# Performance work log

Measured on AMD Instinct MI355X. Metric: run time of the kernel, lower is better.

## Reference

```python
import jax, jax.numpy as jnp
import numpy as np

N_NODES = 100000
N_EDGES = 3200000
IN_DIM = 512
HID_DIM = 512


def setup_inputs() -> dict:
    key = jax.random.key(0)
    k = jax.random.split(key, 8)
    x = jax.random.normal(k[0], (N_NODES, IN_DIM), dtype=jnp.float32)
    adj_src = jax.random.randint(k[1], (N_EDGES,), 0, N_NODES, dtype=jnp.int32)
    adj_dst = jax.random.randint(k[2], (N_EDGES,), 0, N_NODES, dtype=jnp.int32)
    adj_val = jax.random.uniform(k[3], (N_EDGES,), dtype=jnp.float32)
    s = 1.0 / np.sqrt(IN_DIM)
    W1 = jax.random.uniform(k[4], (IN_DIM, HID_DIM), minval=-s, maxval=s, dtype=jnp.float32)
    b1 = jnp.zeros((HID_DIM,), dtype=jnp.float32)
    s2 = 1.0 / np.sqrt(HID_DIM)
    W2 = jax.random.uniform(k[5], (HID_DIM, HID_DIM), minval=-s2, maxval=s2, dtype=jnp.float32)
    b2 = jnp.zeros((HID_DIM,), dtype=jnp.float32)
    return {"x": x, "adj_src": adj_src, "adj_dst": adj_dst, "adj_val": adj_val,
            "W1": W1, "b1": b1, "W2": W2, "b2": b2}


def _spmm(src, dst, val, h):
    # adj @ h with adj in COO: out[dst] += val * h[src]
    msgs = h[src] * val[:, None]            # [E, D]
    return jax.ops.segment_sum(msgs, dst, num_segments=N_NODES)


def reference(x, adj_src, adj_dst, adj_val, W1, b1, W2, b2):
    # Inference mode: dropout is identity (training=False).
    # Layer 1: linear -> SpMM -> ReLU
    h = x @ W1 + b1
    h = _spmm(adj_src, adj_dst, adj_val, h)
    h = jax.nn.relu(h)
    # Layer 2: linear -> SpMM -> ReLU
    h = h @ W2 + b2
    h = _spmm(adj_src, adj_dst, adj_val, h)
    h = jax.nn.relu(h)
    return h
```

## Files before the change

kernel.cpp:

```cpp
#include <hip/hip_runtime.h>


#define N_NODES 100000
#define N_EDGES 3200000
#define DIM 512
#define BUCKET_CAP 128

typedef __attribute__((ext_vector_type(8))) __bf16 bf16x8;
typedef __attribute__((ext_vector_type(4))) float f32x4;
typedef __attribute__((ext_vector_type(4))) unsigned int u32x4;

__device__ inline unsigned short f2bf(float f) {
    unsigned int u = __builtin_bit_cast(unsigned int, f);
    unsigned int r = (u + 0x7FFFu + ((u >> 16) & 1u)) >> 16;
    return (unsigned short)r;
}
__device__ inline float bf2f(unsigned short s) {
    unsigned int u = ((unsigned int)s) << 16;
    return __builtin_bit_cast(float, u);
}

__global__ __launch_bounds__(256) void k_cvt(const float4* __restrict__ in,
                                             ushort4* __restrict__ out, int n4) {
    int i = blockIdx.x * 256 + threadIdx.x;
    if (i >= n4) return;
    float4 v = in[i];
    ushort4 o;
    o.x = f2bf(v.x); o.y = f2bf(v.y); o.z = f2bf(v.z); o.w = f2bf(v.w);
    out[i] = o;
}

__global__ __launch_bounds__(256) void k_wt(const float* __restrict__ W,
                                            unsigned short* __restrict__ Wt) {
    int idx = blockIdx.x * 256 + threadIdx.x;
    int k = idx & 511, n = idx >> 9;
    Wt[n * 512 + k] = f2bf(W[k * 512 + n]);
}

__global__ __launch_bounds__(256) void k_scatter(const int* __restrict__ src,
                                                 const int* __restrict__ dst,
                                                 const float* __restrict__ val,
                                                 int* __restrict__ cnt,
                                                 int2* __restrict__ bucket) {
    int e = blockIdx.x * 256 + threadIdx.x;
    if (e >= N_EDGES) return;
    int d = dst[e];
    int pos = atomicAdd(cnt + d, 1);
    if (pos < BUCKET_CAP)
        bucket[((size_t)d << 7) + pos] = make_int2(src[e], __float_as_int(val[e]));
}

__global__ __launch_bounds__(256, 2)
void k_gemm(const unsigned short* __restrict__ A, const unsigned short* __restrict__ Bt,
            const float* __restrict__ bias, unsigned short* __restrict__ C, int M) {
    __shared__ unsigned short sA[128][40];
    __shared__ unsigned short sB[128][40];
    const int t = threadIdx.x;
    const int m0 = blockIdx.x * 128;
    const int n0 = blockIdx.y * 128;
    const int wave = t >> 6;
    const int lane = t & 63;
    const int wm = (wave & 1) << 6;
    const int wn = (wave >> 1) << 6;
    const int quad = lane >> 4;
    const int l16 = lane & 15;

    f32x4 acc[4][4];
#pragma unroll
    for (int i = 0; i < 4; i++)
#pragma unroll
        for (int j = 0; j < 4; j++) acc[i][j] = (f32x4){0.f, 0.f, 0.f, 0.f};

    const int row_s = t >> 2;
    const int q_s = t & 3;

    for (int k0 = 0; k0 < 512; k0 += 32) {
        __syncthreads();
#pragma unroll
        for (int i = 0; i < 2; i++) {
            int row = row_s + (i << 6);
            int gr = m0 + row;
            u32x4 av = {0u, 0u, 0u, 0u};
            if (gr < M) av = *(const u32x4*)(A + (size_t)gr * 512 + k0 + q_s * 8);
            *(u32x4*)(&sA[row][q_s * 8]) = av;
            u32x4 bv = *(const u32x4*)(Bt + (size_t)(n0 + row) * 512 + k0 + q_s * 8);
            *(u32x4*)(&sB[row][q_s * 8]) = bv;
        }
        __syncthreads();
        bf16x8 af[4], bfr[4];
#pragma unroll
        for (int i = 0; i < 4; i++)
            af[i] = *(const bf16x8*)(&sA[wm + i * 16 + l16][quad * 8]);
#pragma unroll
        for (int j = 0; j < 4; j++)
            bfr[j] = *(const bf16x8*)(&sB[wn + j * 16 + l16][quad * 8]);
#pragma unroll
        for (int i = 0; i < 4; i++)
#pragma unroll
            for (int j = 0; j < 4; j++)
                acc[i][j] = __builtin_amdgcn_mfma_f32_16x16x32_bf16(af[i], bfr[j], acc[i][j], 0, 0, 0);
    }

#pragma unroll
    for (int i = 0; i < 4; i++) {
        int rbase = m0 + wm + i * 16 + quad * 4;
#pragma unroll
        for (int j = 0; j < 4; j++) {
            int col = n0 + wn + j * 16 + l16;
            float bv = bias[col];
#pragma unroll
            for (int r = 0; r < 4; r++) {
                int row = rbase + r;
                if (row < M) C[(size_t)row * 512 + col] = f2bf(acc[i][j][r] + bv);
            }
        }
    }
}

__global__ __launch_bounds__(256)
void k_spmm(const int2* __restrict__ bucket, const int* __restrict__ cnt,
            const unsigned short* __restrict__ Hin,
            unsigned short* __restrict__ out_bf, float* __restrict__ out_f32) {
    __shared__ int2 sE[BUCKET_CAP];
    int node = blockIdx.x;
    int t = threadIdx.x;
    int deg = cnt[node];
    if (deg > BUCKET_CAP) deg = BUCKET_CAP;
    if (t < deg) sE[t] = bucket[((size_t)node << 7) + t];
    __syncthreads();
    float ax = 0.f, ay = 0.f;
    for (int e = 0; e < deg; e++) {
        int2 ed = sE[e];
        float v = __int_as_float(ed.y);
        unsigned int p = *(const unsigned int*)(Hin + ((size_t)ed.x << 9) + (t << 1));
        ax += v * bf2f((unsigned short)(p & 0xFFFFu));
        ay += v * bf2f((unsigned short)(p >> 16));
    }
    ax = fmaxf(ax, 0.f);
    ay = fmaxf(ay, 0.f);
    size_t o = ((size_t)node << 9) + (t << 1);
    if (out_f32 != nullptr) {
        float2 st = make_float2(ax, ay);
        *(float2*)(out_f32 + o) = st;
    } else {
        unsigned int pk = (unsigned int)f2bf(ax) | ((unsigned int)f2bf(ay) << 16);
        *(unsigned int*)(out_bf + o) = pk;
    }
}

extern "C" void kernel_launch(void* const* d_in, const int* in_sizes, int n_in,
                              void* d_out, int out_size, void* d_ws, size_t ws_size,
                              hipStream_t stream) {
    const float* x       = (const float*)d_in[0];
    const int*   adj_src = (const int*)d_in[1];
    const int*   adj_dst = (const int*)d_in[2];
    const float* adj_val = (const float*)d_in[3];
    const float* W1      = (const float*)d_in[4];
    const float* b1      = (const float*)d_in[5];
    const float* W2      = (const float*)d_in[6];
    const float* b2      = (const float*)d_in[7];

    const size_t ND = (size_t)N_NODES * DIM;

    unsigned short* xb  = (unsigned short*)d_ws;
    unsigned short* w1t = xb + ND;
    unsigned short* w2t = w1t + 262144;
    int*  cnt    = (int*)(w2t + 262144);
    int2* bucket = (int2*)(cnt + 100096);

    unsigned short* h1 = (unsigned short*)d_out;
    unsigned short* h2 = h1 + ND;
    unsigned short* h3 = xb;

    k_cvt<<<50000, 256, 0, stream>>>((const float4*)x, (ushort4*)xb, (int)(ND / 4));
    k_wt<<<1024, 256, 0, stream>>>(W1, w1t);
    k_wt<<<1024, 256, 0, stream>>>(W2, w2t);

    hipMemsetAsync(cnt, 0, N_NODES * sizeof(int), stream);
    k_scatter<<<12500, 256, 0, stream>>>(adj_src, adj_dst, adj_val, cnt, bucket);

    dim3 ggrid((N_NODES + 127) / 128, 4);

    k_gemm<<<ggrid, 256, 0, stream>>>(xb, w1t, b1, h1, N_NODES);
    k_spmm<<<N_NODES, 256, 0, stream>>>(bucket, cnt, h1, h2, nullptr);

    k_gemm<<<ggrid, 256, 0, stream>>>(h2, w2t, b2, h3, N_NODES);
    k_spmm<<<N_NODES, 256, 0, stream>>>(bucket, cnt, h3, nullptr, (float*)d_out);
}
```

Baseline: 1.700 ms.

## Map one wave per node in SpMM with 16-byte gathers and nontemporal hints

```diff
diff --git a/kernel.cpp b/kernel.cpp
--- a/kernel.cpp
+++ b/kernel.cpp
@@ -9,6 +9,7 @@
 typedef __attribute__((ext_vector_type(8))) __bf16 bf16x8;
 typedef __attribute__((ext_vector_type(4))) float f32x4;
 typedef __attribute__((ext_vector_type(4))) unsigned int u32x4;
+typedef __attribute__((ext_vector_type(2))) int i32x2;
 
 __device__ inline unsigned short f2bf(float f) {
     unsigned int u = __builtin_bit_cast(unsigned int, f);
@@ -20,13 +21,13 @@
     return __builtin_bit_cast(float, u);
 }
 
-__global__ __launch_bounds__(256) void k_cvt(const float4* __restrict__ in,
+__global__ __launch_bounds__(256) void k_cvt(const f32x4* __restrict__ in,
                                              ushort4* __restrict__ out, int n4) {
     int i = blockIdx.x * 256 + threadIdx.x;
     if (i >= n4) return;
-    float4 v = in[i];
+    f32x4 v = __builtin_nontemporal_load(in + i);
     ushort4 o;
-    o.x = f2bf(v.x); o.y = f2bf(v.y); o.z = f2bf(v.z); o.w = f2bf(v.w);
+    o.x = f2bf(v[0]); o.y = f2bf(v[1]); o.z = f2bf(v[2]); o.w = f2bf(v[3]);
     out[i] = o;
 }
 
@@ -41,13 +42,17 @@
                                                  const int* __restrict__ dst,
                                                  const float* __restrict__ val,
                                                  int* __restrict__ cnt,
-                                                 int2* __restrict__ bucket) {
+                                                 i32x2* __restrict__ bucket) {
     int e = blockIdx.x * 256 + threadIdx.x;
     if (e >= N_EDGES) return;
     int d = dst[e];
     int pos = atomicAdd(cnt + d, 1);
-    if (pos < BUCKET_CAP)
-        bucket[((size_t)d << 7) + pos] = make_int2(src[e], __float_as_int(val[e]));
+    if (pos < BUCKET_CAP) {
+        i32x2 ed;
+        ed[0] = src[e];
+        ed[1] = __float_as_int(val[e]);
+        __builtin_nontemporal_store(ed, bucket + ((size_t)d << 7) + pos);
+    }
 }
 
 __global__ __launch_bounds__(256, 2)
@@ -56,8 +61,8 @@
     __shared__ unsigned short sA[128][40];
     __shared__ unsigned short sB[128][40];
     const int t = threadIdx.x;
-    const int m0 = blockIdx.x * 128;
-    const int n0 = blockIdx.y * 128;
+    const int m0 = blockIdx.y * 128;
+    const int n0 = blockIdx.x * 128;
     const int wave = t >> 6;
     const int lane = t & 63;
     const int wm = (wave & 1) << 6;
@@ -118,33 +123,61 @@
 }
 
 __global__ __launch_bounds__(256)
-void k_spmm(const int2* __restrict__ bucket, const int* __restrict__ cnt,
+void k_spmm(const i32x2* __restrict__ bucket, const int* __restrict__ cnt,
             const unsigned short* __restrict__ Hin,
             unsigned short* __restrict__ out_bf, float* __restrict__ out_f32) {
-    __shared__ int2 sE[BUCKET_CAP];
-    int node = blockIdx.x;
-    int t = threadIdx.x;
+    __shared__ i32x2 sE[4][BUCKET_CAP];
+    const int w = threadIdx.x >> 6;
+    const int lane = threadIdx.x & 63;
+    const int node = blockIdx.x * 4 + w;
     int deg = cnt[node];
     if (deg > BUCKET_CAP) deg = BUCKET_CAP;
-    if (t < deg) sE[t] = bucket[((size_t)node << 7) + t];
+    const i32x2* bk = bucket + ((size_t)node << 7);
+    if (lane < deg)      sE[w][lane]      = __builtin_nontemporal_load(bk + lane);
+    if (lane + 64 < deg) sE[w][lane + 64] = __builtin_nontemporal_load(bk + lane + 64);
     __syncthreads();
-    float ax = 0.f, ay = 0.f;
-    for (int e = 0; e < deg; e++) {
-        int2 ed = sE[e];
-        float v = __int_as_float(ed.y);
-        unsigned int p = *(const unsigned int*)(Hin + ((size_t)ed.x << 9) + (t << 1));
-        ax += v * bf2f((unsigned short)(p & 0xFFFFu));
-        ay += v * bf2f((unsigned short)(p >> 16));
-    }
-    ax = fmaxf(ax, 0.f);
-    ay = fmaxf(ay, 0.f);
-    size_t o = ((size_t)node << 9) + (t << 1);
+
+    float a[8];
+#pragma unroll
+    for (int i = 0; i < 8; i++) a[i] = 0.f;
+
+    if (deg > 0) {
+        i32x2 ed = sE[w][0];
+        float v = __int_as_float(ed[1]);
+        u32x4 p = *(const u32x4*)(Hin + (((size_t)ed[0]) << 9) + (lane << 3));
+        for (int e = 1; e < deg; e++) {
+            i32x2 edn = sE[w][e];
+            float vn = __int_as_float(edn[1]);
+            u32x4 pn = *(const u32x4*)(Hin + (((size_t)edn[0]) << 9) + (lane << 3));
+#pragma unroll
+            for (int q = 0; q < 4; q++) {
+                a[2 * q]     += v * __builtin_bit_cast(float, p[q] << 16);
+                a[2 * q + 1] += v * __builtin_bit_cast(float, p[q] & 0xFFFF0000u);
+            }
+            p = pn; v = vn;
+        }
+#pragma unroll
+        for (int q = 0; q < 4; q++) {
+            a[2 * q]     += v * __builtin_bit_cast(float, p[q] << 16);
+            a[2 * q + 1] += v * __builtin_bit_cast(float, p[q] & 0xFFFF0000u);
+        }
+    }
+
+#pragma unroll
+    for (int i = 0; i < 8; i++) a[i] = fmaxf(a[i], 0.f);
+
+    size_t o = (((size_t)node) << 9) + (lane << 3);
     if (out_f32 != nullptr) {
-        float2 st = make_float2(ax, ay);
-        *(float2*)(out_f32 + o) = st;
+        f32x4 v0 = {a[0], a[1], a[2], a[3]};
+        f32x4 v1 = {a[4], a[5], a[6], a[7]};
+        __builtin_nontemporal_store(v0, (f32x4*)(out_f32 + o));
+        __builtin_nontemporal_store(v1, (f32x4*)(out_f32 + o + 4));
     } else {
-        unsigned int pk = (unsigned int)f2bf(ax) | ((unsigned int)f2bf(ay) << 16);
-        *(unsigned int*)(out_bf + o) = pk;
+        u32x4 pk;
+#pragma unroll
+        for (int q = 0; q < 4; q++)
+            pk[q] = (unsigned int)f2bf(a[2 * q]) | ((unsigned int)f2bf(a[2 * q + 1]) << 16);
+        __builtin_nontemporal_store(pk, (u32x4*)(out_bf + o));
     }
 }
 
@@ -166,24 +199,24 @@
     unsigned short* w1t = xb + ND;
     unsigned short* w2t = w1t + 262144;
     int*  cnt    = (int*)(w2t + 262144);
-    int2* bucket = (int2*)(cnt + 100096);
+    i32x2* bucket = (i32x2*)(cnt + 100096);
 
     unsigned short* h1 = (unsigned short*)d_out;
     unsigned short* h2 = h1 + ND;
     unsigned short* h3 = xb;
 
-    k_cvt<<<50000, 256, 0, stream>>>((const float4*)x, (ushort4*)xb, (int)(ND / 4));
+    k_cvt<<<50000, 256, 0, stream>>>((const f32x4*)x, (ushort4*)xb, (int)(ND / 4));
     k_wt<<<1024, 256, 0, stream>>>(W1, w1t);
     k_wt<<<1024, 256, 0, stream>>>(W2, w2t);
 
     hipMemsetAsync(cnt, 0, N_NODES * sizeof(int), stream);
     k_scatter<<<12500, 256, 0, stream>>>(adj_src, adj_dst, adj_val, cnt, bucket);
 
-    dim3 ggrid((N_NODES + 127) / 128, 4);
+    dim3 ggrid(4, (N_NODES + 127) / 128);
 
     k_gemm<<<ggrid, 256, 0, stream>>>(xb, w1t, b1, h1, N_NODES);
-    k_spmm<<<N_NODES, 256, 0, stream>>>(bucket, cnt, h1, h2, nullptr);
+    k_spmm<<<N_NODES / 4, 256, 0, stream>>>(bucket, cnt, h1, h2, nullptr);
 
     k_gemm<<<ggrid, 256, 0, stream>>>(h2, w2t, b2, h3, N_NODES);
-    k_spmm<<<N_NODES, 256, 0, stream>>>(bucket, cnt, h3, nullptr, (float*)d_out);
-}
+    k_spmm<<<N_NODES / 4, 256, 0, stream>>>(bucket, cnt, h3, nullptr, (float*)d_out);
+}
```

Result: slower. 1.766 ms (+3.9%).

## Fuse fp32-to-bf16 conversion into GEMM loads and double-buffer LDS tiles

Applied to the files above, without the earlier changes.

```diff
diff --git a/kernel.cpp b/kernel.cpp
--- a/kernel.cpp
+++ b/kernel.cpp
@@ -19,15 +19,8 @@
     unsigned int u = ((unsigned int)s) << 16;
     return __builtin_bit_cast(float, u);
 }
-
-__global__ __launch_bounds__(256) void k_cvt(const float4* __restrict__ in,
-                                             ushort4* __restrict__ out, int n4) {
-    int i = blockIdx.x * 256 + threadIdx.x;
-    if (i >= n4) return;
-    float4 v = in[i];
-    ushort4 o;
-    o.x = f2bf(v.x); o.y = f2bf(v.y); o.z = f2bf(v.z); o.w = f2bf(v.w);
-    out[i] = o;
+__device__ inline unsigned int pk2(float a, float b) {
+    return (unsigned int)f2bf(a) | ((unsigned int)f2bf(b) << 16);
 }
 
 __global__ __launch_bounds__(256) void k_wt(const float* __restrict__ W,
@@ -50,14 +43,15 @@
         bucket[((size_t)d << 7) + pos] = make_int2(src[e], __float_as_int(val[e]));
 }
 
+template <int AF32>
 __global__ __launch_bounds__(256, 2)
-void k_gemm(const unsigned short* __restrict__ A, const unsigned short* __restrict__ Bt,
+void k_gemm(const void* __restrict__ Ap, const unsigned short* __restrict__ Bt,
             const float* __restrict__ bias, unsigned short* __restrict__ C, int M) {
-    __shared__ unsigned short sA[128][40];
-    __shared__ unsigned short sB[128][40];
+    __shared__ unsigned short sA[2][128][40];
+    __shared__ unsigned short sB[2][128][40];
     const int t = threadIdx.x;
-    const int m0 = blockIdx.x * 128;
-    const int n0 = blockIdx.y * 128;
+    const int m0 = blockIdx.y * 128;
+    const int n0 = blockIdx.x * 128;
     const int wave = t >> 6;
     const int lane = t & 63;
     const int wm = (wave & 1) << 6;
@@ -73,32 +67,73 @@
 
     const int row_s = t >> 2;
     const int q_s = t & 3;
+    const int eo = q_s * 8;
+
+    const int gr0 = m0 + row_s;
+    const int gr1 = m0 + row_s + 64;
+    const bool ok0 = gr0 < M, ok1 = gr1 < M;
+    const unsigned short* __restrict__ pB0 = Bt + (size_t)(n0 + row_s) * 512 + eo;
+    const unsigned short* __restrict__ pB1 = pB0 + (size_t)64 * 512;
+    const u32x4 zz = (u32x4){0u, 0u, 0u, 0u};
+
+    u32x4 rA0, rA1, rB0, rB1;
+
+    auto ld = [&](int k) {
+        if constexpr (AF32) {
+            const float* A = (const float*)Ap;
+            float4 x0 = {0, 0, 0, 0}, x1 = {0, 0, 0, 0};
+            float4 y0 = {0, 0, 0, 0}, y1 = {0, 0, 0, 0};
+            if (ok0) {
+                const float4* q = (const float4*)(A + (size_t)gr0 * 512 + eo + k);
+                x0 = q[0]; x1 = q[1];
+            }
+            if (ok1) {
+                const float4* q = (const float4*)(A + (size_t)gr1 * 512 + eo + k);
+                y0 = q[0]; y1 = q[1];
+            }
+            rA0[0] = pk2(x0.x, x0.y); rA0[1] = pk2(x0.z, x0.w);
+            rA0[2] = pk2(x1.x, x1.y); rA0[3] = pk2(x1.z, x1.w);
+            rA1[0] = pk2(y0.x, y0.y); rA1[1] = pk2(y0.z, y0.w);
+            rA1[2] = pk2(y1.x, y1.y); rA1[3] = pk2(y1.z, y1.w);
+        } else {
+            const unsigned short* A = (const unsigned short*)Ap;
+            rA0 = ok0 ? *(const u32x4*)(A + (size_t)gr0 * 512 + eo + k) : zz;
+            rA1 = ok1 ? *(const u32x4*)(A + (size_t)gr1 * 512 + eo + k) : zz;
+        }
+        rB0 = *(const u32x4*)(pB0 + k);
+        rB1 = *(const u32x4*)(pB1 + k);
+    };
+    auto st = [&](int buf) {
+        *(u32x4*)(&sA[buf][row_s][eo]) = rA0;
+        *(u32x4*)(&sA[buf][row_s + 64][eo]) = rA1;
+        *(u32x4*)(&sB[buf][row_s][eo]) = rB0;
+        *(u32x4*)(&sB[buf][row_s + 64][eo]) = rB1;
+    };
+
+    ld(0);
+    st(0);
+    ld(32);
+    __syncthreads();
 
     for (int k0 = 0; k0 < 512; k0 += 32) {
-        __syncthreads();
-#pragma unroll
-        for (int i = 0; i < 2; i++) {
-            int row = row_s + (i << 6);
-            int gr = m0 + row;
-            u32x4 av = {0u, 0u, 0u, 0u};
-            if (gr < M) av = *(const u32x4*)(A + (size_t)gr * 512 + k0 + q_s * 8);
-            *(u32x4*)(&sA[row][q_s * 8]) = av;
-            u32x4 bv = *(const u32x4*)(Bt + (size_t)(n0 + row) * 512 + k0 + q_s * 8);
-            *(u32x4*)(&sB[row][q_s * 8]) = bv;
-        }
-        __syncthreads();
+        const int cur = (k0 >> 5) & 1;
         bf16x8 af[4], bfr[4];
 #pragma unroll
         for (int i = 0; i < 4; i++)
-            af[i] = *(const bf16x8*)(&sA[wm + i * 16 + l16][quad * 8]);
+            af[i] = *(const bf16x8*)(&sA[cur][wm + i * 16 + l16][quad * 8]);
 #pragma unroll
         for (int j = 0; j < 4; j++)
-            bfr[j] = *(const bf16x8*)(&sB[wn + j * 16 + l16][quad * 8]);
+            bfr[j] = *(const bf16x8*)(&sB[cur][wn + j * 16 + l16][quad * 8]);
 #pragma unroll
         for (int i = 0; i < 4; i++)
 #pragma unroll
             for (int j = 0; j < 4; j++)
                 acc[i][j] = __builtin_amdgcn_mfma_f32_16x16x32_bf16(af[i], bfr[j], acc[i][j], 0, 0, 0);
+        if (k0 + 32 < 512) {
+            st(cur ^ 1);
+            if (k0 + 64 < 512) ld(k0 + 64);
+            __syncthreads();
+        }
     }
 
 #pragma unroll
@@ -172,18 +207,17 @@
     unsigned short* h2 = h1 + ND;
     unsigned short* h3 = xb;
 
-    k_cvt<<<50000, 256, 0, stream>>>((const float4*)x, (ushort4*)xb, (int)(ND / 4));
     k_wt<<<1024, 256, 0, stream>>>(W1, w1t);
     k_wt<<<1024, 256, 0, stream>>>(W2, w2t);
 
     hipMemsetAsync(cnt, 0, N_NODES * sizeof(int), stream);
     k_scatter<<<12500, 256, 0, stream>>>(adj_src, adj_dst, adj_val, cnt, bucket);
 
-    dim3 ggrid((N_NODES + 127) / 128, 4);
-
-    k_gemm<<<ggrid, 256, 0, stream>>>(xb, w1t, b1, h1, N_NODES);
+    dim3 ggrid(4, (N_NODES + 127) / 128);
+
+    k_gemm<1><<<ggrid, 256, 0, stream>>>((const void*)x, w1t, b1, h1, N_NODES);
     k_spmm<<<N_NODES, 256, 0, stream>>>(bucket, cnt, h1, h2, nullptr);
 
-    k_gemm<<<ggrid, 256, 0, stream>>>(h2, w2t, b2, h3, N_NODES);
+    k_gemm<0><<<ggrid, 256, 0, stream>>>((const void*)h2, w2t, b2, h3, N_NODES);
     k_spmm<<<N_NODES, 256, 0, stream>>>(bucket, cnt, h3, nullptr, (float*)d_out);
 }
```

Result: no change. 1.679 ms (-1.3%).
